# Optimization experiments

Hardware: AMD Instinct MI355X
Metric: run time of the kernel (lower is better)

The kernel has to match this reference:

```python
import jax, jax.numpy as jnp
import numpy as np

NEG_INF = -9e15
ALPHA = 0.2  # LeakyReLU negative slope

N, IN_F, OUT_F = 8192, 512, 64


def setup_inputs() -> dict:
    key = jax.random.key(0)
    k1, k2, k3, k4 = jax.random.split(key, 4)
    input = jax.random.normal(k1, (N, IN_F), dtype=jnp.float32)
    adj = jax.random.randint(k2, (N, N), 0, 2, dtype=jnp.int32)
    init_range = float(np.sqrt(6.0 / (IN_F + OUT_F)))
    W = jax.random.uniform(k3, (IN_F, OUT_F), dtype=jnp.float32,
                           minval=-init_range, maxval=init_range)
    a_range = float(np.sqrt(6.0 / (2 * OUT_F + 1)))
    a = jax.random.uniform(k4, (2 * OUT_F, 1), dtype=jnp.float32,
                           minval=-a_range, maxval=a_range)
    return {"input": input, "adj": adj, "W": W, "a": a}


def reference(input, adj, W, a):
    h = input @ W                      # [N, F']
    a_left, a_right = a[:OUT_F], a[OUT_F:]   # each [F', 1]
    att_l = h @ a_left                 # [N, 1]
    att_r = h @ a_right                # [N, 1]
    e = jax.nn.leaky_relu(att_l + att_r.T, negative_slope=ALPHA)  # [N, N]
    e = jnp.where(adj == 0, jnp.float32(NEG_INF), e)
    attention = jax.nn.softmax(e, axis=1)
    # dropout is identity in eval mode (training=False)
    h_prime = attention @ h            # [N, F']
    return jax.nn.elu(h_prime)         # concat=True -> ELU activation
```

## Files before the change

### kernel.cpp

```cpp
#include <hip/hip_runtime.h>
#include <stdint.h>

#define ALPHA 0.2f
#define LOG2E 1.44269504088896340736f

typedef __attribute__((ext_vector_type(8))) short bf16x8;
typedef __attribute__((ext_vector_type(4))) float f32x4;

__device__ __forceinline__ unsigned short f2bf(float f) {
    unsigned u = __builtin_bit_cast(unsigned, f);
    u += 0x7fffu + ((u >> 16) & 1u);
    return (unsigned short)(u >> 16);
}
__device__ __forceinline__ float bf2f(unsigned short h) {
    unsigned u = ((unsigned)h) << 16;
    return __builtin_bit_cast(float, u);
}
__device__ __forceinline__ unsigned f2ord(float f) {
    unsigned b = __builtin_bit_cast(unsigned, f);
    return (b & 0x80000000u) ? ~b : (b | 0x80000000u);
}
__device__ __forceinline__ float ord2f(unsigned k) {
    unsigned b = (k & 0x80000000u) ? (k & 0x7fffffffu) : ~k;
    return __builtin_bit_cast(float, b);
}

__global__ __launch_bounds__(256) void gat_h(
    const float* __restrict__ input, const float* __restrict__ W,
    float* __restrict__ hPart)
{
    __shared__ float x_lds[16 * 128];
    const int tid = threadIdx.x;
    const int i0  = (blockIdx.x >> 2) * 16;
    const int ks  = blockIdx.x & 3;
    const int k0  = ks * 128;

    {
        const int r  = tid >> 4;
        const int jc = (tid & 15) * 8;
        const float* src = input + (size_t)(i0 + r) * 512 + k0 + jc;
        *(f32x4*)&x_lds[r * 128 + jc]     = *(const f32x4*)src;
        *(f32x4*)&x_lds[r * 128 + jc + 4] = *(const f32x4*)(src + 4);
    }
    __syncthreads();

    const int c = tid & 63;
    const int w = tid >> 6;
    float acc[4] = {0.f, 0.f, 0.f, 0.f};
    const float* Wc = W + (size_t)k0 * 64 + c;
    #pragma unroll 4
    for (int kk = 0; kk < 128; kk += 4) {
        const float w0 = Wc[(kk+0)*64], w1 = Wc[(kk+1)*64];
        const float w2 = Wc[(kk+2)*64], w3 = Wc[(kk+3)*64];
        #pragma unroll
        for (int ri = 0; ri < 4; ++ri) {
            const f32x4 x = *(const f32x4*)&x_lds[(w + 4*ri) * 128 + kk];
            acc[ri] += x.x * w0 + x.y * w1 + x.z * w2 + x.w * w3;
        }
    }
    #pragma unroll
    for (int ri = 0; ri < 4; ++ri)
        hPart[((size_t)ks * 8192 + i0 + w + 4*ri) * 64 + c] = acc[ri];
}

__global__ __launch_bounds__(256) void gat_aux(
    const float* __restrict__ hPart, const float* __restrict__ a,
    float* __restrict__ attL, float* __restrict__ ERt, float* __restrict__ ER2t,
    unsigned short* __restrict__ hPack, unsigned* __restrict__ wsR)
{
    __shared__ float hl[32 * 64];
    __shared__ unsigned rmax;
    const int tid = threadIdx.x;
    const int j0  = blockIdx.x * 32;
    if (tid == 0) rmax = 0u;

    {
        const size_t base = (size_t)j0 * 64 + tid * 8;
        f32x4 s0 = *(const f32x4*)&hPart[base];
        f32x4 s1 = *(const f32x4*)&hPart[base + 4];
        #pragma unroll
        for (int ks = 1; ks < 4; ++ks) {
            const size_t o = (size_t)ks * 524288 + base;
            const f32x4 u0 = *(const f32x4*)&hPart[o];
            const f32x4 u1 = *(const f32x4*)&hPart[o + 4];
            s0.x += u0.x; s0.y += u0.y; s0.z += u0.z; s0.w += u0.w;
            s1.x += u1.x; s1.y += u1.y; s1.z += u1.z; s1.w += u1.w;
        }
        *(f32x4*)&hl[tid * 8]     = s0;
        *(f32x4*)&hl[tid * 8 + 4] = s1;
    }
    __syncthreads();

    {
        const int row = tid >> 3;
        const int cs  = (tid & 7) * 8;
        float pL = 0.f, pR = 0.f;
        #pragma unroll
        for (int u = 0; u < 8; ++u) {
            const float hv = hl[row * 64 + cs + u];
            pL += hv * a[cs + u];
            pR += hv * a[64 + cs + u];
        }
        pL += __shfl_xor(pL, 1, 64); pR += __shfl_xor(pR, 1, 64);
        pL += __shfl_xor(pL, 2, 64); pR += __shfl_xor(pR, 2, 64);
        pL += __shfl_xor(pL, 4, 64); pR += __shfl_xor(pR, 4, 64);
        if ((tid & 7) == 0) {
            attL[j0 + row] = pL;
            ERt [j0 + row] = __builtin_amdgcn_exp2f(pR * LOG2E);
            ER2t[j0 + row] = __builtin_amdgcn_exp2f(ALPHA * pR * LOG2E);
            atomicMax(&rmax, f2ord(pR));
        }
    }

    {
        const int g = tid >> 6;
        const int l = tid & 63;
        const int m = l & 15;
        const int q = l >> 4;
        bf16x8 v;
        #pragma unroll
        for (int u = 0; u < 8; ++u)
            v[u] = (short)f2bf(hl[(q * 8 + u) * 64 + g * 16 + m]);
        *(bf16x8*)&hPack[(size_t)(blockIdx.x * 4 + g) * 512 + l * 8] = v;
    }

    __syncthreads();
    if (tid == 0) atomicMax(wsR, rmax);
}

__global__ __launch_bounds__(256, 8) void gat_attn(
    const int* __restrict__ adj,
    const float* __restrict__ attL, const float* __restrict__ ERt,
    const float* __restrict__ ER2t,
    const unsigned short* __restrict__ hPack, const unsigned* __restrict__ wsR,
    float* __restrict__ pOut, float* __restrict__ lPart)
{
    __shared__ unsigned smem[4096];
    __shared__ float l_lds[64];
    const int tid  = threadIdx.x;
    const int lane = tid & 63;
    const int wq   = tid >> 6;
    const int m    = lane & 15;
    const int quad = lane >> 4;
    const int ti   = blockIdx.x >> 2;
    const int q4   = blockIdx.x & 3;
    const int i0   = ti * 16;
    const int jc0  = q4 * 64 + wq * 16;

    {
        const int r    = tid >> 4;
        const int lidx = (tid & 3) * 16 + r;
        const int t    = (tid & 15) >> 2;
        unsigned char* bb = (unsigned char*)smem;
        const int* src = adj + (size_t)(i0 + r) * 8192 + q4 * 2048 + (tid & 15) * 8;
        #pragma unroll 4
        for (int it = 0; it < 16; ++it) {
            const int4 v0 = *(const int4*)(src + it * 128);
            const int4 v1 = *(const int4*)(src + it * 128 + 4);
            const unsigned b = (unsigned)v0.x + ((unsigned)v0.y << 1)
                             + ((unsigned)v0.z << 2) + ((unsigned)v0.w << 3)
                             + ((unsigned)v1.x << 4) + ((unsigned)v1.y << 5)
                             + ((unsigned)v1.z << 6) + ((unsigned)v1.w << 7);
            bb[((((it >> 2) * 1024) + (it & 3) * 64 + lidx) << 2) + t] = (unsigned char)b;
        }
    }
    __syncthreads();

    unsigned abw[4];
    #pragma unroll
    for (int g4 = 0; g4 < 4; ++g4)
        abw[g4] = smem[wq * 1024 + g4 * 64 + lane];

    const float R   = ord2f(*wsR);
    const float a_l = attL[i0 + m];
    const float t0  = a_l + R;
    const float M   = fmaxf(t0, ALPHA * t0);
    const float mc  = M * LOG2E;
    const float EL  = __builtin_amdgcn_exp2f(__builtin_fmaf(a_l, LOG2E, -mc));
    const float EL2 = __builtin_amdgcn_exp2f(__builtin_fmaf(ALPHA * a_l, LOG2E, -mc));

    const float*          er_p  = ERt  + jc0 * 32 + quad * 8;
    const float*          er2_p = ER2t + jc0 * 32 + quad * 8;
    const unsigned short* hp_p  = hPack + (size_t)jc0 * 4 * 512 + lane * 8;

    f32x4 acc[4];
    #pragma unroll
    for (int g = 0; g < 4; ++g) acc[g] = (f32x4){0.f, 0.f, 0.f, 0.f};
    float lsum = 0.f;

    #pragma unroll
    for (int jg = 0; jg < 4; ++jg) {
        const unsigned ab = abw[jg];
        #pragma unroll
        for (int t = 0; t < 4; ++t) {
            const int s = jg * 4 + t;
            const f32x4 e0  = *(const f32x4*)(er_p  + s * 32);
            const f32x4 e1  = *(const f32x4*)(er_p  + s * 32 + 4);
            const f32x4 f0  = *(const f32x4*)(er2_p + s * 32);
            const f32x4 f1  = *(const f32x4*)(er2_p + s * 32 + 4);
            bf16x8 B[4];
            #pragma unroll
            for (int g = 0; g < 4; ++g)
                B[g] = *(const bf16x8*)(hp_p + (size_t)(s * 4 + g) * 512);

            const unsigned bits = (ab >> (t * 8)) & 0xffu;
            const float ev[8] = { e0.x, e0.y, e0.z, e0.w, e1.x, e1.y, e1.z, e1.w };
            const float fv[8] = { f0.x, f0.y, f0.z, f0.w, f1.x, f1.y, f1.z, f1.w };
            bf16x8 af;
            #pragma unroll
            for (int u = 0; u < 8; ++u) {
                const float p  = fmaxf(EL * ev[u], EL2 * fv[u]);
                const float pv = (bits & (1u << u)) ? p : 0.0f;
                const unsigned short pb = f2bf(pv);
                af[u] = (short)pb;
                lsum += bf2f(pb);
            }
            #pragma unroll
            for (int g = 0; g < 4; ++g)
                acc[g] = __builtin_amdgcn_mfma_f32_16x16x32_bf16(af, B[g], acc[g], 0, 0, 0);
        }
    }

    lsum += __shfl_xor(lsum, 16, 64);
    lsum += __shfl_xor(lsum, 32, 64);
    if (lane < 16) l_lds[wq * 16 + lane] = lsum;
    float* accf = (float*)smem;
    #pragma unroll
    for (int g = 0; g < 4; ++g)
        *(f32x4*)&accf[(wq * 64 + lane) * 16 + g * 4] = acc[g];
    __syncthreads();

    #pragma unroll
    for (int q = 0; q < 4; ++q) {
        const int e      = tid + q * 256;
        const int lane_e = e >> 4;
        const int k16    = e & 15;
        float s = 0.f;
        #pragma unroll
        for (int ww = 0; ww < 4; ++ww) s += accf[(ww * 64 + lane_e) * 16 + k16];
        const int row = (lane_e >> 4) * 4 + (k16 & 3);
        const int col = (k16 >> 2) * 16 + (lane_e & 15);
        pOut[((size_t)q4 * 8192 + i0 + row) * 64 + col] = s;
    }
    if (tid < 16) {
        lPart[q4 * 8192 + i0 + tid] =
            l_lds[tid] + l_lds[16 + tid] + l_lds[32 + tid] + l_lds[48 + tid];
    }
}

__global__ __launch_bounds__(256) void gat_final(
    const float* __restrict__ pOut, const float* __restrict__ lPart,
    float* __restrict__ out)
{
    const int idx = blockIdx.x * 256 + threadIdx.x;
    const int row = idx >> 6;
    const float v = pOut[idx] + pOut[524288 + idx] + pOut[1048576 + idx]
                  + pOut[1572864 + idx];
    const float l = lPart[row] + lPart[8192 + row] + lPart[16384 + row]
                  + lPart[24576 + row];
    const float r = v / l;
    out[idx] = r > 0.f ? r : (__builtin_amdgcn_exp2f(r * LOG2E) - 1.0f);
}

extern "C" void kernel_launch(void* const* d_in, const int* in_sizes, int n_in,
                              void* d_out, int out_size, void* d_ws, size_t ws_size,
                              hipStream_t stream) {
    const float* input = (const float*)d_in[0];
    const int*   adj   = (const int*)d_in[1];
    const float* W     = (const float*)d_in[2];
    const float* a     = (const float*)d_in[3];
    float* out = (float*)d_out;

    char* ws = (char*)d_ws;
    unsigned*       wsR   = (unsigned*)(ws + 0);
    float*          attL  = (float*)(ws + 4096);
    float*          ERt   = (float*)(ws + 36864);
    float*          ER2t  = (float*)(ws + 69632);
    float*          lPart = (float*)(ws + 102400);
    unsigned short* hPack = (unsigned short*)(ws + 262144);
    float*          hPart = (float*)(ws + 2097152);
    float*          pOut  = (float*)(ws + 10485760);

    hipMemsetAsync(d_ws, 0, 64, stream);

    gat_h    <<<2048, 256, 0, stream>>>(input, W, hPart);
    gat_aux  <<< 256, 256, 0, stream>>>(hPart, a, attL, ERt, ER2t, hPack, wsR);
    gat_attn <<<2048, 256, 0, stream>>>(adj, attL, ERt, ER2t, hPack, wsR, pOut, lPart);
    gat_final<<<2048, 256, 0, stream>>>(pOut, lPart, out);
}
```

Measured before the change: 437.4 us.

## Pack adjacency to bitmask in a separate kernel before attention

Adds a gat_pack kernel that streams the int32 adjacency matrix once and writes a 1-bit-per-entry mask to workspace. The attention kernel then reads each row's mask words directly and distributes them with shuffles, dropping its own LDS bit-packing stage and a barrier. The goal is to separate the bandwidth-bound adjacency read from the MFMA-heavy attention kernel so each can run at its own occupancy. The cost is an extra launch and a small extra write and read of the packed mask.

Result: slower. 509.3 us (+16.4%).

```diff
diff --git a/kernel.cpp b/kernel.cpp
--- a/kernel.cpp
+++ b/kernel.cpp
@@ -23,6 +23,31 @@
 __device__ __forceinline__ float ord2f(unsigned k) {
     unsigned b = (k & 0x80000000u) ? (k & 0x7fffffffu) : ~k;
     return __builtin_bit_cast(float, b);
+}
+
+__global__ __launch_bounds__(256) void gat_pack(
+    const int* __restrict__ adj, unsigned* __restrict__ adjU)
+{
+    __shared__ unsigned char nib[2048];
+    const int tid = threadIdx.x;
+    const size_t base = (size_t)blockIdx.x * 8192;
+
+    int4 v[8];
+    #pragma unroll
+    for (int it = 0; it < 8; ++it)
+        v[it] = *(const int4*)&adj[base + it * 1024 + tid * 4];
+    #pragma unroll
+    for (int it = 0; it < 8; ++it)
+        nib[it * 256 + tid] =
+            (unsigned char)(v[it].x + (v[it].y << 1) + (v[it].z << 2) + (v[it].w << 3));
+    __syncthreads();
+
+    const uint2 u = *(const uint2*)&nib[tid * 8];
+    const unsigned w = (u.x & 0xFu)          | ((u.x >> 4) & 0xF0u)
+                     | ((u.x >> 8) & 0xF00u) | ((u.x >> 12) & 0xF000u)
+                     | ((u.y << 16) & 0xF0000u)  | ((u.y << 12) & 0xF00000u)
+                     | ((u.y << 8) & 0xF000000u) | ((u.y << 4) & 0xF0000000u);
+    adjU[blockIdx.x * 256 + tid] = w;
 }
 
 __global__ __launch_bounds__(256) void gat_h(
@@ -129,13 +154,13 @@
 }
 
 __global__ __launch_bounds__(256, 8) void gat_attn(
-    const int* __restrict__ adj,
+    const unsigned* __restrict__ adjU,
     const float* __restrict__ attL, const float* __restrict__ ERt,
     const float* __restrict__ ER2t,
     const unsigned short* __restrict__ hPack, const unsigned* __restrict__ wsR,
     float* __restrict__ pOut, float* __restrict__ lPart)
 {
-    __shared__ unsigned smem[4096];
+    __shared__ float accf[4096];
     __shared__ float l_lds[64];
     const int tid  = threadIdx.x;
     const int lane = tid & 63;
@@ -147,29 +172,9 @@
     const int i0   = ti * 16;
     const int jc0  = q4 * 64 + wq * 16;
 
-    {
-        const int r    = tid >> 4;
-        const int lidx = (tid & 3) * 16 + r;
-        const int t    = (tid & 15) >> 2;
-        unsigned char* bb = (unsigned char*)smem;
-        const int* src = adj + (size_t)(i0 + r) * 8192 + q4 * 2048 + (tid & 15) * 8;
-        #pragma unroll 4
-        for (int it = 0; it < 16; ++it) {
-            const int4 v0 = *(const int4*)(src + it * 128);
-            const int4 v1 = *(const int4*)(src + it * 128 + 4);
-            const unsigned b = (unsigned)v0.x + ((unsigned)v0.y << 1)
-                             + ((unsigned)v0.z << 2) + ((unsigned)v0.w << 3)
-                             + ((unsigned)v1.x << 4) + ((unsigned)v1.y << 5)
-                             + ((unsigned)v1.z << 6) + ((unsigned)v1.w << 7);
-            bb[((((it >> 2) * 1024) + (it & 3) * 64 + lidx) << 2) + t] = (unsigned char)b;
-        }
-    }
-    __syncthreads();
-
-    unsigned abw[4];
-    #pragma unroll
-    for (int g4 = 0; g4 < 4; ++g4)
-        abw[g4] = smem[wq * 1024 + g4 * 64 + lane];
+    const int4 maskv = *(const int4*)&adjU[(size_t)(i0 + m) * 256 + jc0 + quad * 4];
+    const unsigned mk[4] = { (unsigned)maskv.x, (unsigned)maskv.y,
+                             (unsigned)maskv.z, (unsigned)maskv.w };
 
     const float R   = ord2f(*wsR);
     const float a_l = attL[i0 + m];
@@ -189,42 +194,38 @@
     float lsum = 0.f;
 
     #pragma unroll
-    for (int jg = 0; jg < 4; ++jg) {
-        const unsigned ab = abw[jg];
-        #pragma unroll
-        for (int t = 0; t < 4; ++t) {
-            const int s = jg * 4 + t;
-            const f32x4 e0  = *(const f32x4*)(er_p  + s * 32);
-            const f32x4 e1  = *(const f32x4*)(er_p  + s * 32 + 4);
-            const f32x4 f0  = *(const f32x4*)(er2_p + s * 32);
-            const f32x4 f1  = *(const f32x4*)(er2_p + s * 32 + 4);
-            bf16x8 B[4];
-            #pragma unroll
-            for (int g = 0; g < 4; ++g)
-                B[g] = *(const bf16x8*)(hp_p + (size_t)(s * 4 + g) * 512);
-
-            const unsigned bits = (ab >> (t * 8)) & 0xffu;
-            const float ev[8] = { e0.x, e0.y, e0.z, e0.w, e1.x, e1.y, e1.z, e1.w };
-            const float fv[8] = { f0.x, f0.y, f0.z, f0.w, f1.x, f1.y, f1.z, f1.w };
-            bf16x8 af;
-            #pragma unroll
-            for (int u = 0; u < 8; ++u) {
-                const float p  = fmaxf(EL * ev[u], EL2 * fv[u]);
-                const float pv = (bits & (1u << u)) ? p : 0.0f;
-                const unsigned short pb = f2bf(pv);
-                af[u] = (short)pb;
-                lsum += bf2f(pb);
-            }
-            #pragma unroll
-            for (int g = 0; g < 4; ++g)
-                acc[g] = __builtin_amdgcn_mfma_f32_16x16x32_bf16(af, B[g], acc[g], 0, 0, 0);
-        }
+    for (int s = 0; s < 16; ++s) {
+        const unsigned wmask = (unsigned)__shfl((int)mk[s & 3], m + (s >> 2) * 16, 64);
+        const unsigned bits  = (wmask >> (quad * 8)) & 0xffu;
+
+        const f32x4 e0 = *(const f32x4*)(er_p  + s * 32);
+        const f32x4 e1 = *(const f32x4*)(er_p  + s * 32 + 4);
+        const f32x4 f0 = *(const f32x4*)(er2_p + s * 32);
+        const f32x4 f1 = *(const f32x4*)(er2_p + s * 32 + 4);
+        bf16x8 B[4];
+        #pragma unroll
+        for (int g = 0; g < 4; ++g)
+            B[g] = *(const bf16x8*)(hp_p + (size_t)(s * 4 + g) * 512);
+
+        const float ev[8] = { e0.x, e0.y, e0.z, e0.w, e1.x, e1.y, e1.z, e1.w };
+        const float fv[8] = { f0.x, f0.y, f0.z, f0.w, f1.x, f1.y, f1.z, f1.w };
+        bf16x8 af;
+        #pragma unroll
+        for (int u = 0; u < 8; ++u) {
+            const float p  = fmaxf(EL * ev[u], EL2 * fv[u]);
+            const float pv = (bits & (1u << u)) ? p : 0.0f;
+            const unsigned short pb = f2bf(pv);
+            af[u] = (short)pb;
+            lsum += bf2f(pb);
+        }
+        #pragma unroll
+        for (int g = 0; g < 4; ++g)
+            acc[g] = __builtin_amdgcn_mfma_f32_16x16x32_bf16(af, B[g], acc[g], 0, 0, 0);
     }
 
     lsum += __shfl_xor(lsum, 16, 64);
     lsum += __shfl_xor(lsum, 32, 64);
     if (lane < 16) l_lds[wq * 16 + lane] = lsum;
-    float* accf = (float*)smem;
     #pragma unroll
     for (int g = 0; g < 4; ++g)
         *(f32x4*)&accf[(wq * 64 + lane) * 16 + g * 4] = acc[g];
@@ -280,11 +281,13 @@
     unsigned short* hPack = (unsigned short*)(ws + 262144);
     float*          hPart = (float*)(ws + 2097152);
     float*          pOut  = (float*)(ws + 10485760);
+    unsigned*       adjU  = (unsigned*)(ws + 18874368);
 
     hipMemsetAsync(d_ws, 0, 64, stream);
 
+    gat_pack <<<8192, 256, 0, stream>>>(adj, adjU);
     gat_h    <<<2048, 256, 0, stream>>>(input, W, hPart);
     gat_aux  <<< 256, 256, 0, stream>>>(hPart, a, attL, ERt, ER2t, hPack, wsR);
-    gat_attn <<<2048, 256, 0, stream>>>(adj, attL, ERt, ER2t, hPack, wsR, pOut, lPart);
+    gat_attn <<<2048, 256, 0, stream>>>(adjU, attL, ERt, ER2t, hPack, wsR, pOut, lPart);
     gat_final<<<2048, 256, 0, stream>>>(pOut, lPart, out);
 }
```
